# Kernel optimization log

Measured on AMD Instinct MI355X. Metric: run time of the kernel, lower is better.

Reference implementation:

```python
import jax, jax.numpy as jnp
import numpy as np

HIDDEN = 64
INPUT = 19


def _lstm_layer(x, Wih, Whh, bih, bhh):
    # x: [B, T, I]; Wih: [4H, I]; Whh: [4H, H]; biases: [4H]
    B, T, _ = x.shape
    H = Whh.shape[1]
    # Input contribution for all timesteps at once (big GEMM).
    zx = jnp.einsum('bti,gi->btg', x, Wih) + bih + bhh  # [B, T, 4H]

    def step(carry, z_t):
        h, c = carry
        z = z_t + h @ Whh.T  # [B, 4H]
        i, f, g, o = jnp.split(z, 4, axis=-1)  # torch gate order: i, f, g, o
        i = jax.nn.sigmoid(i)
        f = jax.nn.sigmoid(f)
        g = jnp.tanh(g)
        o = jax.nn.sigmoid(o)
        c = f * c + i * g
        h = o * jnp.tanh(c)
        return (h, c), h

    h0 = jnp.zeros((B, H), x.dtype)
    (_, _), hs = jax.lax.scan(step, (h0, h0), jnp.swapaxes(zx, 0, 1))
    return jnp.swapaxes(hs, 0, 1)  # [B, T, H]


def setup_inputs() -> dict:
    key = jax.random.key(0)
    ks = jax.random.split(key, 12)
    B, T = 4096, 168
    s = 1.0 / np.sqrt(HIDDEN)  # torch LSTM/Linear init scale
    u = lambda k, shape: jax.random.uniform(k, shape, jnp.float32, -s, s)
    return {
        'x': jax.random.normal(ks[0], (B, T, INPUT), jnp.float32),
        'Wih0': u(ks[1], (4 * HIDDEN, INPUT)),
        'Whh0': u(ks[2], (4 * HIDDEN, HIDDEN)),
        'bih0': u(ks[3], (4 * HIDDEN,)),
        'bhh0': u(ks[4], (4 * HIDDEN,)),
        'Wih1': u(ks[5], (4 * HIDDEN, HIDDEN)),
        'Whh1': u(ks[6], (4 * HIDDEN, HIDDEN)),
        'bih1': u(ks[7], (4 * HIDDEN,)),
        'bhh1': u(ks[8], (4 * HIDDEN,)),
        'Wfc': u(ks[9], (1, HIDDEN)),
        'bfc': u(ks[10], (1,)),
    }


def reference(x, Wih0, Whh0, bih0, bhh0, Wih1, Whh1, bih1, bhh1, Wfc, bfc):
    h1 = _lstm_layer(x, Wih0, Whh0, bih0, bhh0)   # [B, T, H]
    h2 = _lstm_layer(h1, Wih1, Whh1, bih1, bhh1)  # [B, T, H]
    out = h2[:, -1, :] @ Wfc.T + bfc              # [B, 1]
    return out.squeeze(-1)                        # [B]
```

## Files before the change

### kernel.cpp

```cpp
#include <hip/hip_runtime.h>
#include <math.h>

#define T_STEPS 168
#define INP     19
#define HID     64
#define ROWS    16
#define NTH     512
#define HSTH    72
#define XSTH    40

typedef _Float16 half8   __attribute__((ext_vector_type(8)));
typedef float    floatx4 __attribute__((ext_vector_type(4)));

__device__ __forceinline__ float fast_sigmoid(float x) {
    return __builtin_amdgcn_rcpf(1.0f + __expf(-x));
}
__device__ __forceinline__ float fast_tanh(float x) {
    return 1.0f - 2.0f * __builtin_amdgcn_rcpf(1.0f + __expf(2.0f * x));
}

__global__ __launch_bounds__(NTH) __attribute__((amdgpu_waves_per_eu(2, 2)))
void lstm2_mfma3_kernel(const float* __restrict__ x,
                        const float* __restrict__ Wih0, const float* __restrict__ Whh0,
                        const float* __restrict__ bih0, const float* __restrict__ bhh0,
                        const float* __restrict__ Wih1, const float* __restrict__ Whh1,
                        const float* __restrict__ bih1, const float* __restrict__ bhh1,
                        const float* __restrict__ Wfc,  const float* __restrict__ bfc,
                        float* __restrict__ out)
{
    __shared__ __align__(16) _Float16 xf [2][ROWS][XSTH];
    __shared__ __align__(16) _Float16 h1f[2][ROWS][HSTH];
    __shared__ __align__(16) _Float16 h2f[2][ROWS][HSTH];
    __shared__ float hout[ROWS][HID];

    const int tid  = threadIdx.x;
    const int b0   = blockIdx.x * ROWS;
    const int wv   = tid >> 6;
    const int lane = tid & 63;
    const int quad = lane >> 4;
    const int l16  = lane & 15;
    const int kq   = quad * 8;
    const int lay  = wv >> 2;
    const int uq   = wv & 3;
    const int u    = uq * 16 + l16;

    half8 bfr[4][4];
    float bz[4];
#pragma unroll
    for (int gi = 0; gi < 4; ++gi) {
        const int gr = gi * 64 + u;
        if (lay == 0) {
            const float* wr = Wih0 + gr * INP;
#pragma unroll
            for (int e = 0; e < 8; ++e) {
                const int k = kq + e;
                bfr[gi][0][e] = (k < INP) ? (_Float16)wr[k] : (_Float16)0.0f;
            }
            const float* hr = Whh0 + gr * HID;
#pragma unroll
            for (int e = 0; e < 8; ++e) {
                bfr[gi][1][e] = (_Float16)hr[kq + e];
                bfr[gi][2][e] = (_Float16)hr[32 + kq + e];
            }
            bfr[gi][3] = bfr[gi][2];
            bz[gi] = bih0[gr] + bhh0[gr];
        } else {
            const float* ir = Wih1 + gr * HID;
            const float* hr = Whh1 + gr * HID;
#pragma unroll
            for (int e = 0; e < 8; ++e) {
                bfr[gi][0][e] = (_Float16)ir[kq + e];
                bfr[gi][1][e] = (_Float16)ir[32 + kq + e];
                bfr[gi][2][e] = (_Float16)hr[kq + e];
                bfr[gi][3][e] = (_Float16)hr[32 + kq + e];
            }
            bz[gi] = bih1[gr] + bhh1[gr];
        }
    }

    float cst[4] = {0.f, 0.f, 0.f, 0.f};

    int srr = 0, sii = 0;
    const float* xsrc = nullptr;
    if (tid < ROWS * INP) {
        srr = tid / INP; sii = tid - srr * INP;
        xsrc = x + ((size_t)(b0 + srr) * T_STEPS) * INP + sii;
    }

    for (int e = tid; e < 2 * ROWS * XSTH; e += NTH) ((_Float16*)xf)[e] = (_Float16)0.f;
    for (int e = tid; e < 2 * ROWS * HSTH; e += NTH) {
        ((_Float16*)h1f)[e] = (_Float16)0.f;
        ((_Float16*)h2f)[e] = (_Float16)0.f;
    }
    __syncthreads();
    float xreg = 0.f;
    if (xsrc) {
        xf[0][srr][sii] = (_Float16)xsrc[0];
        xreg = xsrc[INP];
    }
    __syncthreads();

    for (int t = 0; t <= T_STEPS; ++t) {
        float xnew = 0.f;
        if (xsrc) {
            const int tn = (t + 2 < T_STEPS) ? (t + 2) : (T_STEPS - 1);
            xnew = xsrc[(size_t)tn * INP];
        }
        if (xsrc && (t + 1) < T_STEPS)
            xf[(t + 1) & 1][srr][sii] = (_Float16)xreg;

        const bool act = (lay == 0) ? (t < T_STEPS) : (t >= 1);
        if (act) {
            floatx4 acc[4];
#pragma unroll
            for (int gi = 0; gi < 4; ++gi)
                acc[gi] = (floatx4){bz[gi], bz[gi], bz[gi], bz[gi]};
            if (lay == 0) {
                const half8 ax = *(const half8*)&xf [t & 1][l16][kq];
                const half8 a0 = *(const half8*)&h1f[(t + 1) & 1][l16][kq];
                const half8 a1 = *(const half8*)&h1f[(t + 1) & 1][l16][32 + kq];
#pragma unroll
                for (int gi = 0; gi < 4; ++gi) {
                    acc[gi] = __builtin_amdgcn_mfma_f32_16x16x32_f16(ax, bfr[gi][0], acc[gi], 0, 0, 0);
                    acc[gi] = __builtin_amdgcn_mfma_f32_16x16x32_f16(a0, bfr[gi][1], acc[gi], 0, 0, 0);
                    acc[gi] = __builtin_amdgcn_mfma_f32_16x16x32_f16(a1, bfr[gi][2], acc[gi], 0, 0, 0);
                }
            } else {
                const half8 p0 = *(const half8*)&h1f[(t + 1) & 1][l16][kq];
                const half8 p1 = *(const half8*)&h1f[(t + 1) & 1][l16][32 + kq];
                const half8 q0 = *(const half8*)&h2f[t & 1][l16][kq];
                const half8 q1 = *(const half8*)&h2f[t & 1][l16][32 + kq];
#pragma unroll
                for (int gi = 0; gi < 4; ++gi) {
                    acc[gi] = __builtin_amdgcn_mfma_f32_16x16x32_f16(p0, bfr[gi][0], acc[gi], 0, 0, 0);
                    acc[gi] = __builtin_amdgcn_mfma_f32_16x16x32_f16(p1, bfr[gi][1], acc[gi], 0, 0, 0);
                    acc[gi] = __builtin_amdgcn_mfma_f32_16x16x32_f16(q0, bfr[gi][2], acc[gi], 0, 0, 0);
                    acc[gi] = __builtin_amdgcn_mfma_f32_16x16x32_f16(q1, bfr[gi][3], acc[gi], 0, 0, 0);
                }
            }
#pragma unroll
            for (int rg = 0; rg < 4; ++rg) {
                const float ig = fast_sigmoid(acc[0][rg]);
                const float fg = fast_sigmoid(acc[1][rg]);
                const float gg = fast_tanh(acc[2][rg]);
                const float og = fast_sigmoid(acc[3][rg]);
                cst[rg] = fg * cst[rg] + ig * gg;
                const float hv = og * fast_tanh(cst[rg]);
                const int row = quad * 4 + rg;
                if (lay == 0) {
                    h1f[t & 1][row][u] = (_Float16)hv;
                } else {
                    h2f[(t + 1) & 1][row][u] = (_Float16)hv;
                    if (t == T_STEPS) hout[row][u] = hv;
                }
            }
        }
        xreg = xnew;
        __syncthreads();
    }

    if (tid < ROWS) {
        float a = bfc[0];
        const float* hr = hout[tid];
#pragma unroll
        for (int k = 0; k < HID; ++k)
            a = fmaf(hr[k], Wfc[k], a);
        out[b0 + tid] = a;
    }
}

extern "C" void kernel_launch(void* const* d_in, const int* in_sizes, int n_in,
                              void* d_out, int out_size, void* d_ws, size_t ws_size,
                              hipStream_t stream) {
    const float* x    = (const float*)d_in[0];
    const float* Wih0 = (const float*)d_in[1];
    const float* Whh0 = (const float*)d_in[2];
    const float* bih0 = (const float*)d_in[3];
    const float* bhh0 = (const float*)d_in[4];
    const float* Wih1 = (const float*)d_in[5];
    const float* Whh1 = (const float*)d_in[6];
    const float* bih1 = (const float*)d_in[7];
    const float* bhh1 = (const float*)d_in[8];
    const float* Wfc  = (const float*)d_in[9];
    const float* bfc  = (const float*)d_in[10];
    float* out = (float*)d_out;

    const int B = in_sizes[0] / (T_STEPS * INP);
    const int grid = B / ROWS;

    lstm2_mfma3_kernel<<<dim3(grid), dim3(NTH), 0, stream>>>(
        x, Wih0, Whh0, bih0, bhh0, Wih1, Whh1, bih1, bhh1, Wfc, bfc, out);
}
```

Before: 253.2 us.

## Halve rows per block, split gate math across lanes, fuse LSTM cell exps

```diff
diff --git a/kernel.cpp b/kernel.cpp
--- a/kernel.cpp
+++ b/kernel.cpp
@@ -4,7 +4,7 @@
 #define T_STEPS 168
 #define INP     19
 #define HID     64
-#define ROWS    16
+#define ROWS    8
 #define NTH     512
 #define HSTH    72
 #define XSTH    40
@@ -12,15 +12,27 @@
 typedef _Float16 half8   __attribute__((ext_vector_type(8)));
 typedef float    floatx4 __attribute__((ext_vector_type(4)));
 
-__device__ __forceinline__ float fast_sigmoid(float x) {
-    return __builtin_amdgcn_rcpf(1.0f + __expf(-x));
+__device__ __forceinline__ float lstm_cell(float zi, float zf, float zg2,
+                                           float zo, float& c2) {
+    zi  = fminf(fmaxf(zi,  -20.f), 20.f);
+    zf  = fminf(fmaxf(zf,  -20.f), 20.f);
+    zg2 = fminf(fmaxf(zg2, -40.f), 40.f);
+    zo  = fminf(fmaxf(zo,  -20.f), 20.f);
+    const float A = __expf(zi), F = __expf(zf), G = __expf(zg2), O = __expf(zo);
+    const float pA = 1.f + A, pF = 1.f + F, pG = G + 1.f, mG = G - 1.f;
+    const float d   = pA * pG;
+    const float R   = __builtin_amdgcn_rcpf(d * pF);
+    const float ft  = (F * d) * R;
+    const float its = ((A * mG) * pF) * (R * 2.f);
+    c2 = fmaf(ft, c2, its);
+    c2 = fminf(fmaxf(c2, -35.f), 35.f);
+    const float C2 = __expf(c2);
+    const float R2 = __builtin_amdgcn_rcpf((1.f + O) * (C2 + 1.f));
+    return (O * (C2 - 1.f)) * R2;
 }
-__device__ __forceinline__ float fast_tanh(float x) {
-    return 1.0f - 2.0f * __builtin_amdgcn_rcpf(1.0f + __expf(2.0f * x));
-}
-
-__global__ __launch_bounds__(NTH) __attribute__((amdgpu_waves_per_eu(2, 2)))
-void lstm2_mfma3_kernel(const float* __restrict__ x,
+
+__global__ __launch_bounds__(NTH) __attribute__((amdgpu_waves_per_eu(4, 4)))
+void lstm2_mfma4_kernel(const float* __restrict__ x,
                         const float* __restrict__ Wih0, const float* __restrict__ Whh0,
                         const float* __restrict__ bih0, const float* __restrict__ bhh0,
                         const float* __restrict__ Wih1, const float* __restrict__ Whh1,
@@ -28,9 +40,9 @@
                         const float* __restrict__ Wfc,  const float* __restrict__ bfc,
                         float* __restrict__ out)
 {
-    __shared__ __align__(16) _Float16 xf [2][ROWS][XSTH];
-    __shared__ __align__(16) _Float16 h1f[2][ROWS][HSTH];
-    __shared__ __align__(16) _Float16 h2f[2][ROWS][HSTH];
+    __shared__ __align__(16) _Float16 xf [2][16][XSTH];
+    __shared__ __align__(16) _Float16 h1f[2][16][HSTH];
+    __shared__ __align__(16) _Float16 h2f[2][16][HSTH];
     __shared__ float hout[ROWS][HID];
 
     const int tid  = threadIdx.x;
@@ -43,42 +55,45 @@
     const int lay  = wv >> 2;
     const int uq   = wv & 3;
     const int u    = uq * 16 + l16;
+    const bool lowq = (quad < 2);
+    const int rbase = ((lane & 16) ? 4 : 0) + ((lane & 32) ? 2 : 0);
 
     half8 bfr[4][4];
     float bz[4];
 #pragma unroll
     for (int gi = 0; gi < 4; ++gi) {
         const int gr = gi * 64 + u;
+        const float ws = (gi == 2) ? 2.f : 1.f;
         if (lay == 0) {
             const float* wr = Wih0 + gr * INP;
 #pragma unroll
             for (int e = 0; e < 8; ++e) {
                 const int k = kq + e;
-                bfr[gi][0][e] = (k < INP) ? (_Float16)wr[k] : (_Float16)0.0f;
+                bfr[gi][0][e] = (k < INP) ? (_Float16)(ws * wr[k]) : (_Float16)0.0f;
             }
             const float* hr = Whh0 + gr * HID;
 #pragma unroll
             for (int e = 0; e < 8; ++e) {
-                bfr[gi][1][e] = (_Float16)hr[kq + e];
-                bfr[gi][2][e] = (_Float16)hr[32 + kq + e];
+                bfr[gi][1][e] = (_Float16)(ws * hr[kq + e]);
+                bfr[gi][2][e] = (_Float16)(ws * hr[32 + kq + e]);
             }
             bfr[gi][3] = bfr[gi][2];
-            bz[gi] = bih0[gr] + bhh0[gr];
+            bz[gi] = ws * (bih0[gr] + bhh0[gr]);
         } else {
             const float* ir = Wih1 + gr * HID;
             const float* hr = Whh1 + gr * HID;
 #pragma unroll
             for (int e = 0; e < 8; ++e) {
-                bfr[gi][0][e] = (_Float16)ir[kq + e];
-                bfr[gi][1][e] = (_Float16)ir[32 + kq + e];
-                bfr[gi][2][e] = (_Float16)hr[kq + e];
-                bfr[gi][3][e] = (_Float16)hr[32 + kq + e];
-            }
-            bz[gi] = bih1[gr] + bhh1[gr];
+                bfr[gi][0][e] = (_Float16)(ws * ir[kq + e]);
+                bfr[gi][1][e] = (_Float16)(ws * ir[32 + kq + e]);
+                bfr[gi][2][e] = (_Float16)(ws * hr[kq + e]);
+                bfr[gi][3][e] = (_Float16)(ws * hr[32 + kq + e]);
+            }
+            bz[gi] = ws * (bih1[gr] + bhh1[gr]);
         }
     }
 
-    float cst[4] = {0.f, 0.f, 0.f, 0.f};
+    float cstA = 0.f, cstB = 0.f;
 
     int srr = 0, sii = 0;
     const float* xsrc = nullptr;
@@ -87,27 +102,28 @@
         xsrc = x + ((size_t)(b0 + srr) * T_STEPS) * INP + sii;
     }
 
-    for (int e = tid; e < 2 * ROWS * XSTH; e += NTH) ((_Float16*)xf)[e] = (_Float16)0.f;
-    for (int e = tid; e < 2 * ROWS * HSTH; e += NTH) {
+    for (int e = tid; e < 2 * 16 * XSTH; e += NTH) ((_Float16*)xf)[e] = (_Float16)0.f;
+    for (int e = tid; e < 2 * 16 * HSTH; e += NTH) {
         ((_Float16*)h1f)[e] = (_Float16)0.f;
         ((_Float16*)h2f)[e] = (_Float16)0.f;
     }
     __syncthreads();
-    float xreg = 0.f;
+    float xregA = 0.f, xregB = 0.f;
     if (xsrc) {
         xf[0][srr][sii] = (_Float16)xsrc[0];
-        xreg = xsrc[INP];
+        xregA = xsrc[INP];
+        xregB = xsrc[2 * (size_t)INP];
     }
     __syncthreads();
 
     for (int t = 0; t <= T_STEPS; ++t) {
+        if (xsrc && (t + 1) < T_STEPS)
+            xf[(t + 1) & 1][srr][sii] = (_Float16)xregA;
         float xnew = 0.f;
         if (xsrc) {
-            const int tn = (t + 2 < T_STEPS) ? (t + 2) : (T_STEPS - 1);
+            const int tn = (t + 3 < T_STEPS) ? (t + 3) : (T_STEPS - 1);
             xnew = xsrc[(size_t)tn * INP];
         }
-        if (xsrc && (t + 1) < T_STEPS)
-            xf[(t + 1) & 1][srr][sii] = (_Float16)xreg;
 
         const bool act = (lay == 0) ? (t < T_STEPS) : (t >= 1);
         if (act) {
@@ -138,24 +154,29 @@
                     acc[gi] = __builtin_amdgcn_mfma_f32_16x16x32_f16(q1, bfr[gi][3], acc[gi], 0, 0, 0);
                 }
             }
-#pragma unroll
-            for (int rg = 0; rg < 4; ++rg) {
-                const float ig = fast_sigmoid(acc[0][rg]);
-                const float fg = fast_sigmoid(acc[1][rg]);
-                const float gg = fast_tanh(acc[2][rg]);
-                const float og = fast_sigmoid(acc[3][rg]);
-                cst[rg] = fg * cst[rg] + ig * gg;
-                const float hv = og * fast_tanh(cst[rg]);
-                const int row = quad * 4 + rg;
-                if (lay == 0) {
-                    h1f[t & 1][row][u] = (_Float16)hv;
-                } else {
-                    h2f[(t + 1) & 1][row][u] = (_Float16)hv;
-                    if (t == T_STEPS) hout[row][u] = hv;
+            float zA[4], zB[4];
+#pragma unroll
+            for (int gi = 0; gi < 4; ++gi) {
+                const float sA = __shfl_xor(acc[gi][2], 32);
+                const float sB = __shfl_xor(acc[gi][3], 32);
+                zA[gi] = lowq ? acc[gi][0] : sA;
+                zB[gi] = lowq ? acc[gi][1] : sB;
+            }
+            const float hA = lstm_cell(zA[0], zA[1], zA[2], zA[3], cstA);
+            const float hB = lstm_cell(zB[0], zB[1], zB[2], zB[3], cstB);
+            if (lay == 0) {
+                h1f[t & 1][rbase][u]     = (_Float16)hA;
+                h1f[t & 1][rbase + 1][u] = (_Float16)hB;
+            } else {
+                h2f[(t + 1) & 1][rbase][u]     = (_Float16)hA;
+                h2f[(t + 1) & 1][rbase + 1][u] = (_Float16)hB;
+                if (t == T_STEPS) {
+                    hout[rbase][u]     = hA;
+                    hout[rbase + 1][u] = hB;
                 }
             }
         }
-        xreg = xnew;
+        xregA = xregB; xregB = xnew;
         __syncthreads();
     }
 
@@ -188,6 +209,6 @@
     const int B = in_sizes[0] / (T_STEPS * INP);
     const int grid = B / ROWS;
 
-    lstm2_mfma3_kernel<<<dim3(grid), dim3(NTH), 0, stream>>>(
+    lstm2_mfma4_kernel<<<dim3(grid), dim3(NTH), 0, stream>>>(
         x, Wih0, Whh0, bih0, bhh0, Wih1, Whh1, bih1, bhh1, Wfc, bfc, out);
 }
```

New measurement: 308.0 us. 21.6% more time.

## Replace per-step block barrier with per-wave LDS flag synchronization

Applied to the files above, without the earlier changes.

```diff
diff --git a/kernel.cpp b/kernel.cpp
--- a/kernel.cpp
+++ b/kernel.cpp
@@ -20,7 +20,7 @@
 }
 
 __global__ __launch_bounds__(NTH) __attribute__((amdgpu_waves_per_eu(2, 2)))
-void lstm2_mfma3_kernel(const float* __restrict__ x,
+void lstm2_mfma8_kernel(const float* __restrict__ x,
                         const float* __restrict__ Wih0, const float* __restrict__ Whh0,
                         const float* __restrict__ bih0, const float* __restrict__ bhh0,
                         const float* __restrict__ Wih1, const float* __restrict__ Whh1,
@@ -32,6 +32,7 @@
     __shared__ __align__(16) _Float16 h1f[2][ROWS][HSTH];
     __shared__ __align__(16) _Float16 h2f[2][ROWS][HSTH];
     __shared__ float hout[ROWS][HID];
+    __shared__ int   wflags[8 * 8];
 
     const int tid  = threadIdx.x;
     const int b0   = blockIdx.x * ROWS;
@@ -80,11 +81,20 @@
 
     float cst[4] = {0.f, 0.f, 0.f, 0.f};
 
-    int srr = 0, sii = 0;
-    const float* xsrc = nullptr;
-    if (tid < ROWS * INP) {
-        srr = tid / INP; sii = tid - srr * INP;
-        xsrc = x + ((size_t)(b0 + srr) * T_STEPS) * INP + sii;
+    bool stA = false, stB = false;
+    int rA = 0, cA = 0, rB = 0, cB = 0;
+    const float *pA = nullptr, *pB = nullptr;
+    if (lay == 0) {
+        int e = lane;
+        if (e < 4 * INP) {
+            rA = uq * 4 + e / INP; cA = e % INP; stA = true;
+            pA = x + ((size_t)(b0 + rA) * T_STEPS) * INP + cA;
+        }
+        e = lane + 64;
+        if (e < 4 * INP) {
+            rB = uq * 4 + e / INP; cB = e % INP; stB = true;
+            pB = x + ((size_t)(b0 + rB) * T_STEPS) * INP + cB;
+        }
     }
 
     for (int e = tid; e < 2 * ROWS * XSTH; e += NTH) ((_Float16*)xf)[e] = (_Float16)0.f;
@@ -92,24 +102,28 @@
         ((_Float16*)h1f)[e] = (_Float16)0.f;
         ((_Float16*)h2f)[e] = (_Float16)0.f;
     }
+    if (tid < 8) wflags[tid * 8] = 0;
     __syncthreads();
-    float xreg = 0.f;
-    if (xsrc) {
-        xf[0][srr][sii] = (_Float16)xsrc[0];
-        xreg = xsrc[INP];
-    }
+    float xA1 = 0.f, xA2 = 0.f, xB1 = 0.f, xB2 = 0.f;
+    if (stA) { xf[0][rA][cA] = (_Float16)pA[0]; xA1 = pA[INP]; xA2 = pA[2 * (size_t)INP]; }
+    if (stB) { xf[0][rB][cB] = (_Float16)pB[0]; xB1 = pB[INP]; xB2 = pB[2 * (size_t)INP]; }
     __syncthreads();
 
+    volatile int* wf = (volatile int*)wflags;
+
     for (int t = 0; t <= T_STEPS; ++t) {
-        float xnew = 0.f;
-        if (xsrc) {
-            const int tn = (t + 2 < T_STEPS) ? (t + 2) : (T_STEPS - 1);
-            xnew = xsrc[(size_t)tn * INP];
-        }
-        if (xsrc && (t + 1) < T_STEPS)
-            xf[(t + 1) & 1][srr][sii] = (_Float16)xreg;
+        if (lay == 0) {
+            while (wf[0] < t || wf[8] < t || wf[16] < t || wf[24] < t)
+                __builtin_amdgcn_s_sleep(1);
+        } else {
+            while (wf[0]  < t || wf[8]  < t || wf[16] < t || wf[24] < t ||
+                   wf[32] < t || wf[40] < t || wf[48] < t || wf[56] < t)
+                __builtin_amdgcn_s_sleep(1);
+        }
+        asm volatile("" ::: "memory");
 
         const bool act = (lay == 0) ? (t < T_STEPS) : (t >= 1);
+        float hv[4];
         if (act) {
             floatx4 acc[4];
 #pragma unroll
@@ -145,19 +159,46 @@
                 const float gg = fast_tanh(acc[2][rg]);
                 const float og = fast_sigmoid(acc[3][rg]);
                 cst[rg] = fg * cst[rg] + ig * gg;
-                const float hv = og * fast_tanh(cst[rg]);
-                const int row = quad * 4 + rg;
-                if (lay == 0) {
-                    h1f[t & 1][row][u] = (_Float16)hv;
-                } else {
-                    h2f[(t + 1) & 1][row][u] = (_Float16)hv;
-                    if (t == T_STEPS) hout[row][u] = hv;
+                hv[rg]  = og * fast_tanh(cst[rg]);
+            }
+        }
+
+        if (lay == 0) {
+            float nA = 0.f, nB = 0.f;
+            if (stA) {
+                if (t + 1 < T_STEPS) xf[(t + 1) & 1][rA][cA] = (_Float16)xA1;
+                const int tn = (t + 3 < T_STEPS) ? (t + 3) : (T_STEPS - 1);
+                nA = pA[(size_t)tn * INP];
+            }
+            if (stB) {
+                if (t + 1 < T_STEPS) xf[(t + 1) & 1][rB][cB] = (_Float16)xB1;
+                const int tn = (t + 3 < T_STEPS) ? (t + 3) : (T_STEPS - 1);
+                nB = pB[(size_t)tn * INP];
+            }
+            while (wf[32] < t || wf[40] < t || wf[48] < t || wf[56] < t)
+                __builtin_amdgcn_s_sleep(1);
+            asm volatile("" ::: "memory");
+            if (act) {
+#pragma unroll
+                for (int rg = 0; rg < 4; ++rg)
+                    h1f[t & 1][quad * 4 + rg][u] = (_Float16)hv[rg];
+            }
+            xA1 = xA2; xA2 = nA; xB1 = xB2; xB2 = nB;
+        } else {
+            if (act) {
+#pragma unroll
+                for (int rg = 0; rg < 4; ++rg) {
+                    const int row = quad * 4 + rg;
+                    h2f[(t + 1) & 1][row][u] = (_Float16)hv[rg];
+                    if (t == T_STEPS) hout[row][u] = hv[rg];
                 }
             }
         }
-        xreg = xnew;
-        __syncthreads();
-    }
+
+        asm volatile("s_waitcnt lgkmcnt(0)" ::: "memory");
+        if (lane == 0) wf[wv * 8] = t + 1;
+    }
+    __syncthreads();
 
     if (tid < ROWS) {
         float a = bfc[0];
@@ -188,6 +229,6 @@
     const int B = in_sizes[0] / (T_STEPS * INP);
     const int grid = B / ROWS;
 
-    lstm2_mfma3_kernel<<<dim3(grid), dim3(NTH), 0, stream>>>(
+    lstm2_mfma8_kernel<<<dim3(grid), dim3(NTH), 0, stream>>>(
         x, Wih0, Whh0, bih0, bhh0, Wih1, Whh1, bih1, bhh1, Wfc, bfc, out);
 }
```

After: 343.2 us. 1.36x slower.
